# Optimization experiments

Measured on AMD Instinct MI355X. Metric: run time of the kernel, lower is better.

Reference implementation:

```python
import jax, jax.numpy as jnp
import numpy as np

# dims: E experts, B batch, L image tokens, C encoder width, H hidden, Q queries,
# NH heads, O output, NL layers
E, B, L, C, H, Q, NH, O, NL = 4, 8, 768, 1024, 768, 144, 12, 4096, 2
MLP = 4 * H
HD = H // NH
STAGE_Q = (64, 48, 32)     # stage_num default: query tokens per stage
STAGE_L = (256, 256, 256)  # split_part default: image tokens per stage (sum == L)


def _ln(x, w, b, eps=1e-5):
    m = jnp.mean(x, axis=-1, keepdims=True)
    v = jnp.mean((x - m) ** 2, axis=-1, keepdims=True)
    return (x - m) * jax.lax.rsqrt(v + eps) * w + b


def _mha(q, kv, in_w, in_b, out_w, out_b):
    # torch nn.MultiheadAttention math; q: [B,S,H], kv: [B,T,H]
    wq, wk, wv = jnp.split(in_w, 3, axis=1)
    bq, bk, bv = jnp.split(in_b, 3)
    Bq, S = q.shape[0], q.shape[1]
    T = kv.shape[1]
    qh = (q @ wq + bq).reshape(Bq, S, NH, HD)
    kh = (kv @ wk + bk).reshape(Bq, T, NH, HD)
    vh = (kv @ wv + bv).reshape(Bq, T, NH, HD)
    s = jnp.einsum('bqhd,bkhd->bhqk', qh, kh) / np.float32(np.sqrt(HD))
    a = jax.nn.softmax(s, axis=-1)
    o = jnp.einsum('bhqk,bkhd->bqhd', a, vh).reshape(Bq, S, H)
    return o @ out_w + out_b


def _expert(x, in_w, in_b, query, l1w, l1b, lkw, lkb, l2w, l2b,
            aiw, aib, aow, aob, g1, g2, fw, fb, pw, pb, ow, ob):
    # one AttnPooler on gated input x [B,L,C]
    h = x @ in_w + in_b                                     # [B,L,H]
    qt = jnp.broadcast_to(query[None], (x.shape[0], Q, H))  # [B,Q,H]
    q_cuts = np.cumsum(STAGE_Q)[:-1]
    i_cuts = np.cumsum(STAGE_L)[:-1]
    outs = []
    for st, si in zip(jnp.split(qt, q_cuts, axis=1), jnp.split(h, i_cuts, axis=1)):
        kv = jnp.concatenate([st, si], axis=1)  # [B,Sq+Si,H]; fixed across layers
        t = st
        for li in range(NL):
            kvn = _ln(kv, lkw[li], lkb[li])
            qn = _ln(t, l1w[li], l1b[li])
            t = t + g1[li] * _mha(qn, kvn, aiw[li], aib[li], aow[li], aob[li])
            mid = jax.nn.gelu(_ln(t, l2w[li], l2b[li]) @ fw[li] + fb[li], approximate=False)
            t = t + g2[li] * (mid @ pw[li] + pb[li])
        outs.append(t)
    tok = jnp.concatenate(outs, axis=1)  # [B,Q,H]
    return tok @ ow + ob                 # [B,Q,O]


def _forward(image_embs, gate_ln_w, gate_ln_b, gate_w, gate_b,
             exp_in_w, exp_in_b, exp_query,
             ln1_w, ln1_b, ln1kv_w, ln1kv_b, ln2_w, ln2_b,
             attn_in_w, attn_in_b, attn_out_w, attn_out_b,
             ls1, ls2, fc_w, fc_b, proj_w, proj_b, out_w, out_b,
             rms_w, output_gain):
    # gating in fp32 with clamped logits
    x32 = image_embs.astype(jnp.float32)
    logits = jnp.clip(_ln(x32, gate_ln_w, gate_ln_b) @ gate_w + gate_b, -15.0, 15.0)
    w = jax.nn.softmax(logits, axis=-1).astype(image_embs.dtype)        # [B,L,E]
    gated = image_embs[None] * jnp.transpose(w, (2, 0, 1))[..., None]    # [E,B,L,C]
    expert_out = jax.vmap(_expert)(gated, exp_in_w, exp_in_b, exp_query,
                                   ln1_w, ln1_b, ln1kv_w, ln1kv_b, ln2_w, ln2_b,
                                   attn_in_w, attn_in_b, attn_out_w, attn_out_b,
                                   ls1, ls2, fc_w, fc_b, proj_w, proj_b, out_w, out_b)
    mixed = expert_out.sum(axis=0)  # [B,Q,O]
    ms = jnp.mean(mixed ** 2, axis=-1, keepdims=True)  # RMSNorm, eps=1e-6
    return mixed * jax.lax.rsqrt(ms + 1e-6) * rms_w * output_gain


def setup_inputs() -> dict:
    key = jax.random.key(0)
    ks = iter(jax.random.split(key, 32))
    def w(shape, s=0.02):
        return jax.random.normal(next(ks), shape, dtype=jnp.float32) * s
    return {
        'image_embs': jax.random.normal(next(ks), (B, L, C), dtype=jnp.float32),
        'gate_ln_w': jnp.ones((C,), jnp.float32), 'gate_ln_b': jnp.zeros((C,), jnp.float32),
        'gate_w': w((C, E)), 'gate_b': jnp.zeros((E,), jnp.float32),
        'exp_in_w': w((E, C, H)), 'exp_in_b': jnp.zeros((E, H), jnp.float32),
        'exp_query': w((E, Q, H), 0.01),
        'ln1_w': jnp.ones((E, NL, H), jnp.float32), 'ln1_b': jnp.zeros((E, NL, H), jnp.float32),
        'ln1kv_w': jnp.ones((E, NL, H), jnp.float32), 'ln1kv_b': jnp.zeros((E, NL, H), jnp.float32),
        'ln2_w': jnp.ones((E, NL, H), jnp.float32), 'ln2_b': jnp.zeros((E, NL, H), jnp.float32),
        'attn_in_w': w((E, NL, H, 3 * H)), 'attn_in_b': jnp.zeros((E, NL, 3 * H), jnp.float32),
        'attn_out_w': w((E, NL, H, H)), 'attn_out_b': jnp.zeros((E, NL, H), jnp.float32),
        'ls1': jnp.full((E, NL, H), 0.1, jnp.float32), 'ls2': jnp.full((E, NL, H), 0.1, jnp.float32),
        'fc_w': w((E, NL, H, MLP)), 'fc_b': jnp.zeros((E, NL, MLP), jnp.float32),
        'proj_w': w((E, NL, MLP, H)), 'proj_b': jnp.zeros((E, NL, H), jnp.float32),
        'out_w': w((E, H, O)), 'out_b': jnp.zeros((E, O), jnp.float32),
        'rms_w': jnp.ones((O,), jnp.float32),
        'output_gain': jnp.full((O,), 0.3, jnp.float32),
    }


def reference(image_embs, gate_ln_w, gate_ln_b, gate_w, gate_b, exp_in_w, exp_in_b, exp_query, ln1_w, ln1_b, ln1kv_w, ln1kv_b, ln2_w, ln2_b, attn_in_w, attn_in_b, attn_out_w, attn_out_b, ls1, ls2, fc_w, fc_b, proj_w, proj_b, out_w, out_b, rms_w, output_gain):
    return _forward(image_embs, gate_ln_w, gate_ln_b, gate_w, gate_b, exp_in_w, exp_in_b, exp_query, ln1_w, ln1_b, ln1kv_w, ln1kv_b, ln2_w, ln2_b, attn_in_w, attn_in_b, attn_out_w, attn_out_b, ls1, ls2, fc_w, fc_b, proj_w, proj_b, out_w, out_b, rms_w, output_gain)
```

## Files before the change

kernel.cpp:

```cpp
#include <hip/hip_runtime.h>

typedef __attribute__((ext_vector_type(4))) float f4;
typedef __attribute__((ext_vector_type(8))) __bf16 bf16x8;
typedef __attribute__((ext_vector_type(4))) __bf16 bf16x4;
typedef __attribute__((ext_vector_type(4))) unsigned short u16x4;


#define GLD16(gp, lp)                                                        \
  __builtin_amdgcn_global_load_lds(                                          \
      (__attribute__((address_space(1))) void*)(gp),                         \
      (__attribute__((address_space(3))) void*)(lp), 16, 0, 0)

__global__ __launch_bounds__(256) void gate_kernel(
    const float* __restrict__ x, const float* __restrict__ lnw,
    const float* __restrict__ lnb, const float* __restrict__ gwm,
    const float* __restrict__ gb, float* __restrict__ out) {
  const long r = blockIdx.x;
  const int tid = threadIdx.x;
  f4 v = *(const f4*)(x + r * 1024 + tid * 4);
  float s1 = v[0] + v[1] + v[2] + v[3];
  float s2 = v[0]*v[0] + v[1]*v[1] + v[2]*v[2] + v[3]*v[3];
#pragma unroll
  for (int off = 32; off; off >>= 1) { s1 += __shfl_down(s1, off); s2 += __shfl_down(s2, off); }
  __shared__ float red[8];
  const int wv = tid >> 6;
  if ((tid & 63) == 0) { red[wv*2] = s1; red[wv*2+1] = s2; }
  __syncthreads();
  const float sum = red[0]+red[2]+red[4]+red[6];
  const float sq  = red[1]+red[3]+red[5]+red[7];
  const float mean = sum * (1.f/1024.f);
  const float var  = sq * (1.f/1024.f) - mean*mean;
  const float rstd = rsqrtf(var + 1e-5f);
  f4 lw = *(const f4*)(lnw + tid*4);
  f4 lb = *(const f4*)(lnb + tid*4);
  f4 acc = {0.f,0.f,0.f,0.f};
#pragma unroll
  for (int i = 0; i < 4; i++) {
    float n = (v[i]-mean)*rstd*lw[i] + lb[i];
    f4 g = *(const f4*)(gwm + (long)(tid*4+i)*4);
    acc += n * g;
  }
#pragma unroll
  for (int off = 32; off; off >>= 1) {
    acc[0] += __shfl_down(acc[0], off); acc[1] += __shfl_down(acc[1], off);
    acc[2] += __shfl_down(acc[2], off); acc[3] += __shfl_down(acc[3], off);
  }
  __shared__ f4 red4[4];
  if ((tid & 63) == 0) red4[wv] = acc;
  __syncthreads();
  if (tid == 0) {
    f4 tot = red4[0] + red4[1] + red4[2] + red4[3];
    float lg[4], mx = -1e30f;
#pragma unroll
    for (int e = 0; e < 4; e++) {
      float tv = tot[e] + gb[e];
      tv = fminf(15.f, fmaxf(-15.f, tv));
      lg[e] = tv; mx = fmaxf(mx, tv);
    }
    float den = 0.f;
#pragma unroll
    for (int e = 0; e < 4; e++) { float ev = __expf(lg[e]-mx); lg[e] = ev; den += ev; }
    const float inv = 1.f/den;
    f4 o;
#pragma unroll
    for (int e = 0; e < 4; e++) o[e] = lg[e]*inv;
    *(f4*)(out + r*4) = o;
  }
}

__global__ __launch_bounds__(256) void transpose_cvt(
    const float* __restrict__ src, __bf16* __restrict__ dst,
    int srcLd, int K, long srcZ, long dstZ) {
  __shared__ float tile[32][33];
  const long so = (long)blockIdx.z * srcZ;
  const long dxo = (long)blockIdx.z * dstZ;
  const int n0 = blockIdx.x * 32, k0 = blockIdx.y * 32;
  const int tx = threadIdx.x & 31, ty = threadIdx.x >> 5;
#pragma unroll
  for (int i = ty; i < 32; i += 8)
    tile[i][tx] = src[so + (long)(k0 + i) * srcLd + n0 + tx];
  __syncthreads();
#pragma unroll
  for (int i = ty; i < 32; i += 8)
    dst[dxo + (long)(n0 + i) * K + k0 + tx] = (__bf16)tile[tx][i];
}

__global__ __launch_bounds__(256) void cvt_bf16_kernel(
    const float* __restrict__ in, __bf16* __restrict__ out) {
  const long i = ((long)blockIdx.x * 256 + threadIdx.x) * 4;
  f4 v = *(const f4*)(in + i);
  bf16x4 o;
  o[0] = (__bf16)v[0]; o[1] = (__bf16)v[1]; o[2] = (__bf16)v[2]; o[3] = (__bf16)v[3];
  *(bf16x4*)(out + i) = o;
}

__global__ __launch_bounds__(256) void zero_f32_kernel(float* __restrict__ p) {
  const long i = ((long)blockIdx.x * 256 + threadIdx.x) * 4;
  *(f4*)(p + i) = (f4){0.f, 0.f, 0.f, 0.f};
}

__global__ __launch_bounds__(256) void ln_rows_kernel(
    const float* __restrict__ in, __bf16* __restrict__ out,
    const float* __restrict__ w, const float* __restrict__ b) {
  const long r = blockIdx.x;
  const int e = (int)(r / 1152);
  const float* src = in + r * 768;
  const int tid = threadIdx.x;
  float v0 = src[tid], v1 = src[tid+256], v2 = src[tid+512];
  float s1 = v0+v1+v2, s2 = v0*v0+v1*v1+v2*v2;
#pragma unroll
  for (int off = 32; off; off >>= 1) { s1 += __shfl_down(s1, off); s2 += __shfl_down(s2, off); }
  __shared__ float red[8];
  const int wv = tid >> 6;
  if ((tid & 63) == 0) { red[wv*2] = s1; red[wv*2+1] = s2; }
  __syncthreads();
  const float sum = red[0]+red[2]+red[4]+red[6];
  const float sq  = red[1]+red[3]+red[5]+red[7];
  const float mean = sum * (1.f/768.f);
  const float var  = sq * (1.f/768.f) - mean*mean;
  const float rstd = rsqrtf(var + 1e-5f);
  const float* wp = w + (long)e * 1536;
  const float* bp = b + (long)e * 1536;
  __bf16* dst = out + r * 768;
  dst[tid]     = (__bf16)((v0-mean)*rstd*wp[tid]     + bp[tid]);
  dst[tid+256] = (__bf16)((v1-mean)*rstd*wp[tid+256] + bp[tid+256]);
  dst[tid+512] = (__bf16)((v2-mean)*rstd*wp[tid+512] + bp[tid+512]);
}

__global__ __launch_bounds__(256) void ln_kv_kernel(
    const __bf16* __restrict__ h, const float* __restrict__ query,
    __bf16* __restrict__ out, const float* __restrict__ w, const float* __restrict__ b,
    int T, int Sq, int qoffG, int loff) {
  const long r = blockIdx.x;
  const int e = (int)(r / (8*T));
  const int rem = (int)(r % (8*T));
  const int bb = rem / T;
  const int p = rem % T;
  const int tid = threadIdx.x;
  float v0, v1, v2;
  if (p < Sq) {
    const float* src = query + ((long)e * 144 + qoffG + p) * 768;
    v0 = src[tid]; v1 = src[tid+256]; v2 = src[tid+512];
  } else {
    const __bf16* src = h + (((long)e * 8 + bb) * 768 + loff + (p - Sq)) * 768;
    v0 = (float)src[tid]; v1 = (float)src[tid+256]; v2 = (float)src[tid+512];
  }
  float s1 = v0+v1+v2, s2 = v0*v0+v1*v1+v2*v2;
#pragma unroll
  for (int off = 32; off; off >>= 1) { s1 += __shfl_down(s1, off); s2 += __shfl_down(s2, off); }
  __shared__ float red[8];
  const int wv = tid >> 6;
  if ((tid & 63) == 0) { red[wv*2] = s1; red[wv*2+1] = s2; }
  __syncthreads();
  const float sum = red[0]+red[2]+red[4]+red[6];
  const float sq  = red[1]+red[3]+red[5]+red[7];
  const float mean = sum * (1.f/768.f);
  const float var  = sq * (1.f/768.f) - mean*mean;
  const float rstd = rsqrtf(var + 1e-5f);
  const float* wp = w + (long)e * 1536;
  const float* bp2 = b + (long)e * 1536;
  __bf16* dst = out + r * 768;
  dst[tid]     = (__bf16)((v0-mean)*rstd*wp[tid]     + bp2[tid]);
  dst[tid+256] = (__bf16)((v1-mean)*rstd*wp[tid+256] + bp2[tid+256]);
  dst[tid+512] = (__bf16)((v2-mean)*rstd*wp[tid+512] + bp2[tid+512]);
}

__global__ __launch_bounds__(256) void init_t_kernel(
    const float* __restrict__ query, float* __restrict__ t) {
  const long i4 = ((long)blockIdx.x * 256 + threadIdx.x) * 4;
  const int e = (int)(i4 / 884736);
  const int rq = (int)(i4 % 110592);
  *(f4*)(t + i4) = *(const f4*)(query + (long)e * 110592 + rq);
}

struct GemmP {
  const __bf16* A; long sAz; int lda;
  const __bf16* Bt; long sBz; int ldb;
  void* C; long sCz; int ldc;
  const float* bias; long sBiasZ;
  const float* vec; long sVecZ;
  int K;
};

template<int MODE, bool C_BF16>
__global__ __launch_bounds__(256) void gemm128(GemmP p) {
  __shared__ __bf16 As[2][128][32];
  __shared__ __bf16 Bs[2][128][32];
  const int z = blockIdx.z;
  int e = z, koff = 0, KK = p.K;
  if (MODE == 5) { e = z >> 1; }
  if (MODE == 6) { e = z & 3; KK = p.K >> 1; koff = (z >> 2) * KK; }

  const __bf16* Ab = p.A + (long)e * p.sAz + koff;
  const __bf16* Bb = p.Bt + (long)(MODE == 5 ? z : e) * p.sBz + koff;
  const float* bias = p.bias + (long)(MODE == 5 ? z : e) * p.sBiasZ;
  const float* vec = (MODE == 4 || MODE == 6) ? (p.vec + (long)e * p.sVecZ) : nullptr;

  const int m0 = blockIdx.x * 128, n0 = blockIdx.y * 128;
  const int tid = threadIdx.x;
  const int w = tid >> 6, lane = tid & 63;
  const int lr = lane & 15, qd = lane >> 4;
  const int wm = (w & 1) * 64, wn = (w >> 1) * 64;

  const int sr = w * 32 + (lane >> 2);
  const int sc = (lane & 3) * 8;
  const int lda = p.lda, ldb = p.ldb;
  const __bf16* gA = Ab + (long)(m0 + sr) * lda + sc;
  const __bf16* gB = Bb + (long)(n0 + sr) * ldb + sc;

  f4 acc[4][4];
#pragma unroll
  for (int i = 0; i < 4; i++)
#pragma unroll
    for (int j = 0; j < 4; j++) acc[i][j] = (f4){0.f, 0.f, 0.f, 0.f};

  const int nk = KK >> 5;

#define STAGE(buf, t)                                        \
  do {                                                       \
    const __bf16* a_ = gA + (long)(t) * 32;                  \
    const __bf16* b_ = gB + (long)(t) * 32;                  \
    GLD16(a_,                 &As[buf][w * 32][0]);          \
    GLD16(a_ + 16 * lda,      &As[buf][w * 32 + 16][0]);     \
    GLD16(b_,                 &Bs[buf][w * 32][0]);          \
    GLD16(b_ + 16 * ldb,      &Bs[buf][w * 32 + 16][0]);     \
  } while (0)

  STAGE(0, 0);
  __syncthreads();
  int cur = 0;
  for (int t = 0; t < nk; ++t) {
    if (t + 1 < nk) STAGE(cur ^ 1, t + 1);
    bf16x8 af[4], bfr[4];
#pragma unroll
    for (int i = 0; i < 4; i++) af[i] = *(const bf16x8*)&As[cur][wm + i*16 + lr][qd*8];
#pragma unroll
    for (int j = 0; j < 4; j++) bfr[j] = *(const bf16x8*)&Bs[cur][wn + j*16 + lr][qd*8];
#pragma unroll
    for (int i = 0; i < 4; i++)
#pragma unroll
      for (int j = 0; j < 4; j++)
        acc[i][j] = __builtin_amdgcn_mfma_f32_16x16x32_bf16(af[i], bfr[j], acc[i][j], 0, 0, 0);
    __syncthreads();
    cur ^= 1;
  }
#undef STAGE

  long cOff;
  if (MODE == 5)      cOff = (long)(z & 1) * 2048;
  else if (MODE == 6) cOff = (long)e * p.sCz;
  else                cOff = (long)z * p.sCz;
  float* Cf = (float*)p.C + cOff;
  __bf16* Cb = (__bf16*)p.C + cOff;
#pragma unroll
  for (int i = 0; i < 4; i++) {
    const int rbase = m0 + wm + i*16 + qd*4;
#pragma unroll
    for (int j = 0; j < 4; j++) {
      const int col = n0 + wn + j*16 + lr;
      const float bcol = bias[col];
      f4 v = acc[i][j];
#pragma unroll
      for (int r = 0; r < 4; r++) {
        const long o = (long)(rbase + r) * p.ldc + col;
        const float xx = v[r];
        if (MODE == 0) {
          const float y = xx + bcol;
          if (C_BF16) Cb[o] = (__bf16)y; else Cf[o] = y;
        } else if (MODE == 1) {
          const float y = xx + bcol;
          const float g = 0.5f * y * (1.0f + erff(y * 0.70710678118654752f));
          if (C_BF16) Cb[o] = (__bf16)g; else Cf[o] = g;
        } else if (MODE == 4) {
          const float y = vec[(long)(rbase + r) * 4 + z] * xx + bcol;
          if (C_BF16) Cb[o] = (__bf16)y; else Cf[o] = y;
        } else if (MODE == 5) {
          unsafeAtomicAdd(&Cf[o], xx + bcol);
        } else if (MODE == 6) {
          unsafeAtomicAdd(&Cf[o], vec[col] * (xx + (koff == 0 ? bcol : 0.f)));
        }
      }
    }
  }
}

template<int TSQ, int TT>
__global__ __launch_bounds__(256) void attn_mfma_kernel(
    const __bf16* __restrict__ qh, const __bf16* __restrict__ kvh,
    __bf16* __restrict__ att, int qoffG) {
  constexpr int MT = TSQ / 16;
  constexpr int NT = TT / 16;
  constexpr int NC = (TT + 31) / 32;
  constexpr int TC = NC * 32;
  constexpr int TPAD = 328;
  __shared__ __bf16 Plds[64 * TPAD];
  __shared__ unsigned Vt32[64 * 20];
  __shared__ float redf[64 * 4];

  const int hh = blockIdx.x;
  const long eb = blockIdx.y;
  const int tid = threadIdx.x;
  const int w = tid >> 6, lane = tid & 63, lr = lane & 15, qd = lane >> 4;

  const __bf16* qb = qh + ((long)eb * 144 + qoffG) * 768 + hh * 64;
  const __bf16* kb = kvh + (long)eb * TT * 1536 + hh * 64;
  const __bf16* vb = kb + 768;

  bf16x8 qf[MT][2];
#pragma unroll
  for (int mt = 0; mt < MT; mt++)
#pragma unroll
    for (int kc = 0; kc < 2; kc++)
      qf[mt][kc] = *(const bf16x8*)(qb + (long)(mt*16 + lr)*768 + kc*32 + qd*8);

  f4 sacc[MT][5];
#pragma unroll
  for (int mt = 0; mt < MT; mt++)
#pragma unroll
    for (int j = 0; j < 5; j++) sacc[mt][j] = (f4){0.f,0.f,0.f,0.f};
#pragma unroll
  for (int j = 0; j < 5; j++) {
    const int jj = w + 4*j;
    if (jj < NT) {
      const int t0 = jj * 16;
      bf16x8 kf0 = *(const bf16x8*)(kb + (long)(t0 + lr)*1536 + qd*8);
      bf16x8 kf1 = *(const bf16x8*)(kb + (long)(t0 + lr)*1536 + 32 + qd*8);
#pragma unroll
      for (int mt = 0; mt < MT; mt++) {
        sacc[mt][j] = __builtin_amdgcn_mfma_f32_16x16x32_bf16(qf[mt][0], kf0, sacc[mt][j], 0,0,0);
        sacc[mt][j] = __builtin_amdgcn_mfma_f32_16x16x32_bf16(qf[mt][1], kf1, sacc[mt][j], 0,0,0);
      }
    }
  }

  float rowmax[MT][4], linv[MT][4], ps[MT][4];
#pragma unroll
  for (int mt = 0; mt < MT; mt++)
#pragma unroll
    for (int r = 0; r < 4; r++) {
      float m = -1e30f;
#pragma unroll
      for (int j = 0; j < 5; j++)
        if (w + 4*j < NT) m = fmaxf(m, sacc[mt][j][r]);
#pragma unroll
      for (int d = 1; d < 16; d <<= 1) m = fmaxf(m, __shfl_xor(m, d));
      rowmax[mt][r] = m;
    }
  if (lr == 0) {
#pragma unroll
    for (int mt = 0; mt < MT; mt++)
#pragma unroll
      for (int r = 0; r < 4; r++)
        redf[(mt*16 + qd*4 + r)*4 + w] = rowmax[mt][r];
  }
  __syncthreads();
#pragma unroll
  for (int mt = 0; mt < MT; mt++)
#pragma unroll
    for (int r = 0; r < 4; r++) {
      f4 v = *(const f4*)&redf[(mt*16 + qd*4 + r)*4];
      rowmax[mt][r] = fmaxf(fmaxf(v[0],v[1]), fmaxf(v[2],v[3])) * 0.125f;
      ps[mt][r] = 0.f;
    }

#pragma unroll
  for (int j = 0; j < 5; j++) {
    const int jj = w + 4*j;
    if (jj < NT) {
#pragma unroll
      for (int mt = 0; mt < MT; mt++)
#pragma unroll
        for (int r = 0; r < 4; r++) {
          float e = __expf(sacc[mt][j][r]*0.125f - rowmax[mt][r]);
          ps[mt][r] += e;
          Plds[(mt*16 + qd*4 + r)*TPAD + jj*16 + lr] = (__bf16)e;
        }
    }
  }
#pragma unroll
  for (int mt = 0; mt < MT; mt++)
#pragma unroll
    for (int r = 0; r < 4; r++) {
      float s = ps[mt][r];
#pragma unroll
      for (int d = 1; d < 16; d <<= 1) s += __shfl_xor(s, d);
      ps[mt][r] = s;
    }
  __syncthreads();
  if (lr == 0) {
#pragma unroll
    for (int mt = 0; mt < MT; mt++)
#pragma unroll
      for (int r = 0; r < 4; r++)
        redf[(mt*16 + qd*4 + r)*4 + w] = ps[mt][r];
  }
  if (TC > TT) {
    for (int idx = tid; idx < 64*(TC-TT); idx += 256) {
      const int rr = idx / (TC-TT), cc = idx % (TC-TT);
      Plds[rr*TPAD + TT + cc] = (__bf16)0.f;
    }
  }
  __syncthreads();
#pragma unroll
  for (int mt = 0; mt < MT; mt++)
#pragma unroll
    for (int r = 0; r < 4; r++) {
      f4 v = *(const f4*)&redf[(mt*16 + qd*4 + r)*4];
      linv[mt][r] = 1.f / (v[0]+v[1]+v[2]+v[3]);
    }

  f4 oacc[MT];
#pragma unroll
  for (int mt = 0; mt < MT; mt++) oacc[mt] = (f4){0.f,0.f,0.f,0.f};
  const int n0 = w * 16;
  for (int c = 0; c < NC; c++) {
    {
      const int tp = tid & 15, dq = tid >> 4;
      const int t0v = c*32 + tp*2;
      u16x4 v0 = (u16x4){0,0,0,0}, v1 = (u16x4){0,0,0,0};
      if (t0v < TT)     v0 = *(const u16x4*)(vb + (long)t0v*1536 + dq*4);
      if (t0v + 1 < TT) v1 = *(const u16x4*)(vb + (long)(t0v+1)*1536 + dq*4);
#pragma unroll
      for (int i = 0; i < 4; i++)
        Vt32[(dq*4 + i)*20 + tp] = ((unsigned)v1[i] << 16) | (unsigned)v0[i];
    }
    __syncthreads();
    bf16x8 vf = *(const bf16x8*)&Vt32[(n0 + lr)*20 + qd*4];
#pragma unroll
    for (int mt = 0; mt < MT; mt++) {
      bf16x8 pf = *(const bf16x8*)&Plds[(mt*16 + lr)*TPAD + c*32 + qd*8];
      oacc[mt] = __builtin_amdgcn_mfma_f32_16x16x32_bf16(pf, vf, oacc[mt], 0,0,0);
    }
    __syncthreads();
  }

  __bf16* ob = att + ((long)eb*144 + qoffG)*768 + hh*64 + n0 + lr;
#pragma unroll
  for (int mt = 0; mt < MT; mt++)
#pragma unroll
    for (int r = 0; r < 4; r++) {
      const int row = mt*16 + qd*4 + r;
      ob[(long)row * 768] = (__bf16)(oacc[mt][r] * linv[mt][r]);
    }
}

__global__ __launch_bounds__(256) void rmsnorm_kernel(
    const float* __restrict__ in, const float* __restrict__ w,
    const float* __restrict__ g, float* __restrict__ out) {
  const long r = blockIdx.x;
  const int tid = threadIdx.x;
  const float* src = in + r*4096;
  f4 vv[4]; float s2 = 0.f;
#pragma unroll
  for (int i = 0; i < 4; i++) {
    vv[i] = *(const f4*)(src + i*1024 + tid*4);
    s2 += vv[i][0]*vv[i][0] + vv[i][1]*vv[i][1] + vv[i][2]*vv[i][2] + vv[i][3]*vv[i][3];
  }
#pragma unroll
  for (int off = 32; off; off >>= 1) s2 += __shfl_down(s2, off);
  __shared__ float red[4];
  if ((tid & 63) == 0) red[tid >> 6] = s2;
  __syncthreads();
  const float ms = (red[0]+red[1]+red[2]+red[3]) * (1.f/4096.f);
  const float scl = rsqrtf(ms + 1e-6f);
#pragma unroll
  for (int i = 0; i < 4; i++) {
    const int o = i*1024 + tid*4;
    f4 wv = *(const f4*)(w + o);
    f4 gv = *(const f4*)(g + o);
    f4 res = vv[i] * scl * wv * gv;
    *(f4*)(out + r*4096 + o) = res;
  }
}

extern "C" void kernel_launch(void* const* d_in, const int* in_sizes, int n_in,
                              void* d_out, int out_size, void* d_ws, size_t ws_size,
                              hipStream_t stream) {
  const float* x          = (const float*)d_in[0];
  const float* gate_ln_w  = (const float*)d_in[1];
  const float* gate_ln_b  = (const float*)d_in[2];
  const float* gate_w     = (const float*)d_in[3];
  const float* gate_b     = (const float*)d_in[4];
  const float* exp_in_w   = (const float*)d_in[5];
  const float* exp_in_b   = (const float*)d_in[6];
  const float* exp_query  = (const float*)d_in[7];
  const float* ln1_w      = (const float*)d_in[8];
  const float* ln1_b      = (const float*)d_in[9];
  const float* ln1kv_w    = (const float*)d_in[10];
  const float* ln1kv_b    = (const float*)d_in[11];
  const float* ln2_w      = (const float*)d_in[12];
  const float* ln2_b      = (const float*)d_in[13];
  const float* attn_in_w  = (const float*)d_in[14];
  const float* attn_in_b  = (const float*)d_in[15];
  const float* attn_out_w = (const float*)d_in[16];
  const float* attn_out_b = (const float*)d_in[17];
  const float* ls1        = (const float*)d_in[18];
  const float* ls2        = (const float*)d_in[19];
  const float* fc_w       = (const float*)d_in[20];
  const float* fc_b       = (const float*)d_in[21];
  const float* proj_w     = (const float*)d_in[22];
  const float* proj_b     = (const float*)d_in[23];
  const float* out_w      = (const float*)d_in[24];
  const float* out_b      = (const float*)d_in[25];
  const float* rms_w      = (const float*)d_in[26];
  const float* out_gain   = (const float*)d_in[27];
  float* out = (float*)d_out;

  char* W = (char*)d_ws;
  float*   gw     = (float*)(W + 0);
  float*   t      = (float*)(W + 98304);
  __bf16*  qn     = (__bf16*)(W + 14254080);
  __bf16*  tb     = (__bf16*)(W + 14254080);
  __bf16*  qh     = (__bf16*)(W + 21331968);
  __bf16*  kvn    = (__bf16*)(W + 28409856);
  __bf16*  kvh    = (__bf16*)(W + 44138496);
  __bf16*  mid    = (__bf16*)(W + 44138496);
  __bf16*  outw_t = (__bf16*)(W + 44138496);
  __bf16*  h      = (__bf16*)(W + 75595776);
  float*   mixed  = (float*)(W + 75595776);
  __bf16*  wbuf   = (__bf16*)(W + 113344512);
  __bf16*  xb     = (__bf16*)(W + 119635968);
  const size_t NEED = 132218880ull;
  if (ws_size < NEED) return;

  cvt_bf16_kernel<<<6144, 256, 0, stream>>>(x, xb);
  gate_kernel<<<6144, 256, 0, stream>>>(x, gate_ln_w, gate_ln_b, gate_w, gate_b, gw);

  transpose_cvt<<<dim3(24,32,4), 256, 0, stream>>>(exp_in_w, wbuf, 768, 1024, 786432, 786432);
  { GemmP p{ xb, 0, 1024, wbuf, 786432, 1024, h, 4718592, 768,
             exp_in_b, 768, gw, 0, 1024 };
    gemm128<4,true><<<dim3(48,6,4), 256, 0, stream>>>(p); }
  init_t_kernel<<<3456, 256, 0, stream>>>(exp_query, t);

  const int ST[3]  = {320, 304, 288};
  const int SQ[3]  = {64, 48, 32};
  const int QO[3]  = {0, 64, 112};
  const int LO[3]  = {0, 256, 512};

  for (int li = 0; li < 2; li++) {
    transpose_cvt<<<dim3(72,24,4), 256, 0, stream>>>(
        attn_in_w + (long)li*768*2304, wbuf, 2304, 768, 3538944, 1769472);
    ln_rows_kernel<<<4608, 256, 0, stream>>>(t, qn, ln1_w + li*768, ln1_b + li*768);
    { GemmP p{ qn, 884736, 768, wbuf, 1769472, 768, qh, 884736, 768,
               attn_in_b + li*2304, 4608, nullptr, 0, 768 };
      gemm128<0,true><<<dim3(9,6,4), 256, 0, stream>>>(p); }
    for (int s = 0; s < 3; s++) {
      const int T = ST[s];
      ln_kv_kernel<<<32*T, 256, 0, stream>>>(h, exp_query, kvn,
          ln1kv_w + li*768, ln1kv_b + li*768, T, SQ[s], QO[s], LO[s]);
      { GemmP p{ kvn, (long)8*T*768, 768, wbuf + 768*768, 1769472, 768,
                 kvh, (long)8*T*1536, 1536,
                 attn_in_b + li*2304 + 768, 4608, nullptr, 0, 768 };
        gemm128<0,true><<<dim3(8*T/128,12,4), 256, 0, stream>>>(p); }
      if (s == 0)
        attn_mfma_kernel<64,320><<<dim3(12,32), 256, 0, stream>>>(qh, kvh, qn, QO[s]);
      else if (s == 1)
        attn_mfma_kernel<48,304><<<dim3(12,32), 256, 0, stream>>>(qh, kvh, qn, QO[s]);
      else
        attn_mfma_kernel<32,288><<<dim3(12,32), 256, 0, stream>>>(qh, kvh, qn, QO[s]);
    }
    transpose_cvt<<<dim3(24,24,4), 256, 0, stream>>>(
        attn_out_w + (long)li*589824, wbuf, 768, 768, 1179648, 589824);
    { GemmP p{ qn , 884736, 768, wbuf, 589824, 768, t, 884736, 768,
               attn_out_b + li*768, 1536, ls1 + li*768, 1536, 768 };
      gemm128<6,false><<<dim3(9,6,8), 256, 0, stream>>>(p); }
    ln_rows_kernel<<<4608, 256, 0, stream>>>(t, qn, ln2_w + li*768, ln2_b + li*768);
    transpose_cvt<<<dim3(96,24,4), 256, 0, stream>>>(
        fc_w + (long)li*768*3072, wbuf, 3072, 768, 4718592, 2359296);
    { GemmP p{ qn, 884736, 768, wbuf, 2359296, 768, mid, 3538944, 3072,
               fc_b + li*3072, 6144, nullptr, 0, 768 };
      gemm128<1,true><<<dim3(9,24,4), 256, 0, stream>>>(p); }
    transpose_cvt<<<dim3(24,96,4), 256, 0, stream>>>(
        proj_w + (long)li*3072*768, wbuf, 768, 3072, 4718592, 2359296);
    { GemmP p{ mid, 3538944, 3072, wbuf, 2359296, 3072, t, 884736, 768,
               proj_b + li*768, 1536, ls2 + li*768, 1536, 3072 };
      gemm128<6,false><<<dim3(9,6,8), 256, 0, stream>>>(p); }
  }

  cvt_bf16_kernel<<<3456, 256, 0, stream>>>(t, tb);
  zero_f32_kernel<<<4608, 256, 0, stream>>>(mixed);
  transpose_cvt<<<dim3(128,24,4), 256, 0, stream>>>(out_w, outw_t, 4096, 768, 3145728, 3145728);
  { GemmP p{ tb, 884736, 768, outw_t, 1572864, 768, mixed, 0, 4096,
             out_b, 2048, nullptr, 0, 768 };
    gemm128<5,false><<<dim3(9,16,8), 256, 0, stream>>>(p); }
  rmsnorm_kernel<<<1152, 256, 0, stream>>>(mixed, rms_w, out_gain, out);
}
```

Measured before the change: 1.452 ms.

## Concatenate experts along K for output GEMM and fuse input bf16 cast into gate

The final expert-sum projection becomes a single GEMM with K=3072. The four expert token tensors are concatenated along K and the output weights are stacked, with the four biases pre-summed. This replaces the split atomic-add GEMM and the zero-fill kernel. Separately, the fp32-to-bf16 conversion of the input is folded into the gate kernel, which removes one full read of x. The trade-off is that the single-z GEMM launches fewer blocks (9x32 instead of 9x16x8), so occupancy may drop.

```diff
diff --git a/kernel.cpp b/kernel.cpp
--- a/kernel.cpp
+++ b/kernel.cpp
@@ -14,10 +14,14 @@
 __global__ __launch_bounds__(256) void gate_kernel(
     const float* __restrict__ x, const float* __restrict__ lnw,
     const float* __restrict__ lnb, const float* __restrict__ gwm,
-    const float* __restrict__ gb, float* __restrict__ out) {
+    const float* __restrict__ gb, float* __restrict__ out,
+    __bf16* __restrict__ xb) {
   const long r = blockIdx.x;
   const int tid = threadIdx.x;
   f4 v = *(const f4*)(x + r * 1024 + tid * 4);
+  bf16x4 xo;
+  xo[0] = (__bf16)v[0]; xo[1] = (__bf16)v[1]; xo[2] = (__bf16)v[2]; xo[3] = (__bf16)v[3];
+  *(bf16x4*)(xb + r * 1024 + tid * 4) = xo;
   float s1 = v[0] + v[1] + v[2] + v[3];
   float s2 = v[0]*v[0] + v[1]*v[1] + v[2]*v[2] + v[3]*v[3];
 #pragma unroll
@@ -85,18 +89,22 @@
     dst[dxo + (long)(n0 + i) * K + k0 + tx] = (__bf16)tile[tx][i];
 }
 
-__global__ __launch_bounds__(256) void cvt_bf16_kernel(
-    const float* __restrict__ in, __bf16* __restrict__ out) {
-  const long i = ((long)blockIdx.x * 256 + threadIdx.x) * 4;
-  f4 v = *(const f4*)(in + i);
-  bf16x4 o;
-  o[0] = (__bf16)v[0]; o[1] = (__bf16)v[1]; o[2] = (__bf16)v[2]; o[3] = (__bf16)v[3];
-  *(bf16x4*)(out + i) = o;
-}
-
-__global__ __launch_bounds__(256) void zero_f32_kernel(float* __restrict__ p) {
-  const long i = ((long)blockIdx.x * 256 + threadIdx.x) * 4;
-  *(f4*)(p + i) = (f4){0.f, 0.f, 0.f, 0.f};
+__global__ __launch_bounds__(256) void cvt_tcat_kernel(
+    const float* __restrict__ t, __bf16* __restrict__ o) {
+  const long i4 = ((long)blockIdx.x * 256 + threadIdx.x) * 4;
+  const int e = (int)(i4 / 884736);
+  const int rem = (int)(i4 % 884736);
+  const int m = rem / 768, k = rem % 768;
+  f4 v = *(const f4*)(t + i4);
+  bf16x4 w;
+  w[0] = (__bf16)v[0]; w[1] = (__bf16)v[1]; w[2] = (__bf16)v[2]; w[3] = (__bf16)v[3];
+  *(bf16x4*)(o + (long)m * 3072 + e * 768 + k) = w;
+}
+
+__global__ __launch_bounds__(256) void bias_sum_kernel(
+    const float* __restrict__ b, float* __restrict__ o) {
+  const int i = blockIdx.x * 256 + threadIdx.x;
+  o[i] = b[i] + b[4096 + i] + b[8192 + i] + b[12288 + i];
 }
 
 __global__ __launch_bounds__(256) void ln_rows_kernel(
@@ -188,12 +196,11 @@
   __shared__ __bf16 Bs[2][128][32];
   const int z = blockIdx.z;
   int e = z, koff = 0, KK = p.K;
-  if (MODE == 5) { e = z >> 1; }
   if (MODE == 6) { e = z & 3; KK = p.K >> 1; koff = (z >> 2) * KK; }
 
   const __bf16* Ab = p.A + (long)e * p.sAz + koff;
-  const __bf16* Bb = p.Bt + (long)(MODE == 5 ? z : e) * p.sBz + koff;
-  const float* bias = p.bias + (long)(MODE == 5 ? z : e) * p.sBiasZ;
+  const __bf16* Bb = p.Bt + (long)e * p.sBz + koff;
+  const float* bias = p.bias + (long)e * p.sBiasZ;
   const float* vec = (MODE == 4 || MODE == 6) ? (p.vec + (long)e * p.sVecZ) : nullptr;
 
   const int m0 = blockIdx.x * 128, n0 = blockIdx.y * 128;
@@ -246,10 +253,7 @@
   }
 #undef STAGE
 
-  long cOff;
-  if (MODE == 5)      cOff = (long)(z & 1) * 2048;
-  else if (MODE == 6) cOff = (long)e * p.sCz;
-  else                cOff = (long)z * p.sCz;
+  const long cOff = (MODE == 6) ? (long)e * p.sCz : (long)z * p.sCz;
   float* Cf = (float*)p.C + cOff;
   __bf16* Cb = (__bf16*)p.C + cOff;
 #pragma unroll
@@ -274,8 +278,6 @@
         } else if (MODE == 4) {
           const float y = vec[(long)(rbase + r) * 4 + z] * xx + bcol;
           if (C_BF16) Cb[o] = (__bf16)y; else Cf[o] = y;
-        } else if (MODE == 5) {
-          unsafeAtomicAdd(&Cf[o], xx + bcol);
         } else if (MODE == 6) {
           unsafeAtomicAdd(&Cf[o], vec[col] * (xx + (koff == 0 ? bcol : 0.f)));
         }
@@ -508,14 +510,15 @@
 
   char* W = (char*)d_ws;
   float*   gw     = (float*)(W + 0);
+  float*   bsum   = (float*)(W + 0);
   float*   t      = (float*)(W + 98304);
   __bf16*  qn     = (__bf16*)(W + 14254080);
-  __bf16*  tb     = (__bf16*)(W + 14254080);
+  __bf16*  tbcat  = (__bf16*)(W + 14254080);
   __bf16*  qh     = (__bf16*)(W + 21331968);
   __bf16*  kvn    = (__bf16*)(W + 28409856);
   __bf16*  kvh    = (__bf16*)(W + 44138496);
   __bf16*  mid    = (__bf16*)(W + 44138496);
-  __bf16*  outw_t = (__bf16*)(W + 44138496);
+  __bf16*  outwc  = (__bf16*)(W + 44138496);
   __bf16*  h      = (__bf16*)(W + 75595776);
   float*   mixed  = (float*)(W + 75595776);
   __bf16*  wbuf   = (__bf16*)(W + 113344512);
@@ -523,8 +526,7 @@
   const size_t NEED = 132218880ull;
   if (ws_size < NEED) return;
 
-  cvt_bf16_kernel<<<6144, 256, 0, stream>>>(x, xb);
-  gate_kernel<<<6144, 256, 0, stream>>>(x, gate_ln_w, gate_ln_b, gate_w, gate_b, gw);
+  gate_kernel<<<6144, 256, 0, stream>>>(x, gate_ln_w, gate_ln_b, gate_w, gate_b, gw, xb);
 
   transpose_cvt<<<dim3(24,32,4), 256, 0, stream>>>(exp_in_w, wbuf, 768, 1024, 786432, 786432);
   { GemmP p{ xb, 0, 1024, wbuf, 786432, 1024, h, 4718592, 768,
@@ -577,11 +579,11 @@
       gemm128<6,false><<<dim3(9,6,8), 256, 0, stream>>>(p); }
   }
 
-  cvt_bf16_kernel<<<3456, 256, 0, stream>>>(t, tb);
-  zero_f32_kernel<<<4608, 256, 0, stream>>>(mixed);
-  transpose_cvt<<<dim3(128,24,4), 256, 0, stream>>>(out_w, outw_t, 4096, 768, 3145728, 3145728);
-  { GemmP p{ tb, 884736, 768, outw_t, 1572864, 768, mixed, 0, 4096,
-             out_b, 2048, nullptr, 0, 768 };
-    gemm128<5,false><<<dim3(9,16,8), 256, 0, stream>>>(p); }
+  cvt_tcat_kernel<<<3456, 256, 0, stream>>>(t, tbcat);
+  bias_sum_kernel<<<16, 256, 0, stream>>>(out_b, bsum);
+  transpose_cvt<<<dim3(128,24,4), 256, 0, stream>>>(out_w, outwc, 4096, 3072, 3145728, 768);
+  { GemmP p{ tbcat, 0, 3072, outwc, 0, 3072, mixed, 0, 4096,
+             bsum, 0, nullptr, 0, 3072 };
+    gemm128<0,false><<<dim3(9,32,1), 256, 0, stream>>>(p); }
   rmsnorm_kernel<<<1152, 256, 0, stream>>>(mixed, rms_w, out_gain, out);
 }
```

After: 1.416 ms. -2.5%, faster.
